# Kernel tuning notes

Hardware: AMD Instinct MI355X
Metric: run time of the kernel (lower is better)

The kernel has to match this reference:

```python
import jax, jax.numpy as jnp
import numpy as np
import math

B, C, A, W, H = 8, 128, 16, 64, 64


def setup_inputs() -> dict:
    key = jax.random.key(0)
    ks = jax.random.split(key, 7)
    s_in = 1.0 / math.sqrt(C)
    return {
        "x": jax.random.normal(ks[0], (B, C, W, H), dtype=jnp.float32),
        "Wq": jax.random.normal(ks[1], (A, C), dtype=jnp.float32) * s_in,
        "bq": jnp.zeros((A,), dtype=jnp.float32),
        "Wk": jax.random.normal(ks[2], (A, C), dtype=jnp.float32) * s_in,
        "bk": jnp.zeros((A,), dtype=jnp.float32),
        "Wv": jax.random.normal(ks[3], (C, C), dtype=jnp.float32) * s_in,
        "bv": jnp.zeros((C,), dtype=jnp.float32),
    }


def reference(x, Wq, bq, Wk, bk, Wv, bv):
    # 1x1 convs == per-pixel linear projections
    q = jnp.einsum('ac,bcwh->bawh', Wq, x) + bq[None, :, None, None]  # [B,A,W,H]
    k = jnp.einsum('ac,bcwh->bawh', Wk, x) + bk[None, :, None, None]  # [B,A,W,H]
    v = jnp.einsum('vc,bcwh->bvwh', Wv, x) + bv[None, :, None, None]  # [B,C,W,H]

    scale = 1.0 / math.sqrt(q.shape[1])
    # full spatial attention: [B, W, H, W, H]
    attn = jnp.einsum('bawh,baWH->bwhWH', q, k)
    b, w, h, _, _ = attn.shape
    attn = jax.nn.softmax(attn.reshape(b, w, h, -1) * scale, axis=-1)
    attn = attn.reshape(b, w, h, w, h)
    out = jnp.einsum('bwhWH,bvWH->bvwh', attn, v)  # [B,C,W,H]
    return out
```

## Files before the change

kernel.cpp:

```cpp
#include <hip/hip_runtime.h>
#include <math.h>

#define BB 8
#define CC 128
#define NN 4096

typedef _Float16 f16;
typedef _Float16 f16x4v __attribute__((ext_vector_type(4)));
typedef _Float16 f16x8 __attribute__((ext_vector_type(8)));
typedef float f32x4v __attribute__((ext_vector_type(4)));
typedef float f32x16 __attribute__((ext_vector_type(16)));

#if __has_builtin(__builtin_amdgcn_exp2f)
#define EXP2(x) __builtin_amdgcn_exp2f(x)
#else
#define EXP2(x) __expf((x)*0.69314718056f)
#endif

#define QSCALE 0.360673760222f
#define SHIFT  5.770780163555f

#define WF_BYTES 65536

__global__ __launch_bounds__(256)
void prep_kernel(const float* __restrict__ Wq, const float* __restrict__ bq,
                 const float* __restrict__ Wk, const float* __restrict__ bk,
                 const float* __restrict__ Wv, const float* __restrict__ bv,
                 f16* __restrict__ Wf, float* __restrict__ biasS)
{
    const int tg = blockIdx.x*256 + threadIdx.x;
    if (tg < 2560) {
        const int mt = tg >> 9, ks = (tg >> 6) & 7, l = tg & 63;
        const int n32 = l & 31, h = l >> 5;
        const int r = mt*32 + n32;
        f16x8 v8;
        #pragma unroll
        for (int i = 0; i < 8; i++) {
            int c = ks*16 + 8*h + i;
            float wv_;
            if (r < 16)      wv_ = QSCALE * Wq[r*CC + c];
            else if (r < 32) wv_ = Wk[(r-16)*CC + c];
            else             wv_ = Wv[(r-32)*CC + c];
            v8[i] = (f16)wv_;
        }
        *(f16x8*)&Wf[(size_t)tg*8] = v8;
    }
    if (blockIdx.x == 0 && threadIdx.x < 160) {
        int r = threadIdx.x;
        biasS[r] = r < 16 ? QSCALE*bq[r] : (r < 32 ? bk[r-16] : bv[r-32]);
    }
}

__global__ __launch_bounds__(256)
void proj_kernel(const float* __restrict__ x, const f16* __restrict__ Wf,
                 const float* __restrict__ biasS,
                 f16* __restrict__ Qt, f16* __restrict__ Kt, f16* __restrict__ Vf)
{
    __shared__ __align__(16) f16 Vl[CC*140];

    const int tid  = threadIdx.x;
    const int lane = tid & 63;
    const int wv   = tid >> 6;
    const int b    = blockIdx.x & 7;
    const int pt   = blockIdx.x >> 3;
    const int n32  = lane & 31;
    const int half = lane >> 5;
    const int p    = pt*128 + wv*32 + n32;

    const float* xp = x + (size_t)b*CC*NN + p;
    f16x8 xf[8];
    #pragma unroll
    for (int ks = 0; ks < 8; ks++) {
        float xv[8];
        #pragma unroll
        for (int i = 0; i < 8; i++)
            xv[i] = __builtin_nontemporal_load(&xp[(size_t)(ks*16 + 8*half + i)*NN]);
        #pragma unroll
        for (int i = 0; i < 8; i++) xf[ks][i] = (f16)xv[i];
    }

    f32x16 acc[5];
    #pragma unroll
    for (int mt = 0; mt < 5; mt++) acc[mt] = (f32x16)0.0f;
    #pragma unroll
    for (int ks = 0; ks < 8; ks++) {
        #pragma unroll
        for (int mt = 0; mt < 5; mt++) {
            f16x8 wfr = *(const f16x8*)&Wf[((size_t)(mt*8 + ks)*64 + lane)*8];
            acc[mt] = __builtin_amdgcn_mfma_f32_32x32x16_f16(wfr, xf[ks], acc[mt], 0, 0, 0);
        }
    }

    #pragma unroll
    for (int mt = 0; mt < 5; mt++) {
        #pragma unroll
        for (int q = 0; q < 4; q++) {
            float4 b4 = *(const float4*)&biasS[mt*32 + q*8 + 4*half];
            acc[mt][q*4+0] += b4.x; acc[mt][q*4+1] += b4.y;
            acc[mt][q*4+2] += b4.z; acc[mt][q*4+3] += b4.w;
        }
    }

    {
        size_t qkoff = ((size_t)b*NN + p)*16;
        f16x4v s0, s1, s2, s3;
        #pragma unroll
        for (int i = 0; i < 4; i++) {
            s0[i] = (f16)acc[0][i];    s1[i] = (f16)acc[0][4+i];
            s2[i] = (f16)acc[0][8+i];  s3[i] = (f16)acc[0][12+i];
        }
        *(f16x4v*)&Qt[qkoff + 4*half]     = s0;
        *(f16x4v*)&Qt[qkoff + 8 + 4*half] = s1;
        *(f16x4v*)&Kt[qkoff + 4*half]     = s2;
        *(f16x4v*)&Kt[qkoff + 8 + 4*half] = s3;
    }

    #pragma unroll
    for (int mt = 1; mt < 5; mt++) {
        #pragma unroll
        for (int g = 0; g < 16; g++) {
            int c = (mt-1)*32 + (g & 3) + 8*(g >> 2) + 4*half;
            Vl[c*140 + wv*32 + n32] = (f16)acc[mt][g];
        }
    }
    __syncthreads();

    #pragma unroll
    for (int pass = 0; pass < 8; pass++) {
        int item = pass*256 + tid;
        int l    = item & 63;
        int f    = (item >> 6) & 15;
        int ktl  = item >> 10;
        int c16  = f >> 2, ct = f & 3;
        int li   = l & 31, h2 = l >> 5;
        const f16* src = &Vl[(ct*32 + li)*140 + ktl*64 + c16*16 + 4*h2];
        f16x4v lo = *(const f16x4v*)&src[0];
        f16x4v hi = *(const f16x4v*)&src[8];
        f16x8 v8;
        #pragma unroll
        for (int i = 0; i < 4; i++) { v8[i] = lo[i]; v8[4+i] = hi[i]; }
        int ktg = pt*2 + ktl;
        *(f16x8*)&Vf[((((size_t)b*64 + ktg)*16 + c16*4 + ct)*64 + l)*8] = v8;
    }
}

__global__ __launch_bounds__(256, 2)
void attn_kernel(const f16* __restrict__ Qt, const f16* __restrict__ Kt,
                 const f16* __restrict__ Vf, float* __restrict__ out)
{
    __shared__ __align__(16) unsigned char lds_raw[53504];

    const int tid  = threadIdx.x;
    const int lane = tid & 63;
    const int w    = tid >> 6;
    const int cp   = w & 1;
    const int kh   = w >> 1;
    const int b    = blockIdx.x & 7;
    const int qt   = blockIdx.x >> 3;
    const int q0   = qt*64;
    const int n32  = lane & 31;
    const int half = lane >> 5;

    const f16* vb = Vf + (size_t)b*64*16*512;
    const f16* kb = Kt + (size_t)b*NN*16;
    const f16x8 qf = *(const f16x8*)&Qt[((size_t)b*NN + q0 + cp*32 + n32)*16 + half*8];

    f32x16 ofA[2], ofB[2];
    #pragma unroll
    for (int c = 0; c < 2; c++) { ofA[c] = (f32x16)0.0f; ofB[c] = (f32x16)0.0f; }
    float ps[4] = {0.f, 0.f, 0.f, 0.f};

    f16x8 kf0 = *(const f16x8*)&kb[((size_t)kh*64 + n32)*16 + half*8];
    f16x8 kf1 = *(const f16x8*)&kb[((size_t)kh*64 + 32 + n32)*16 + half*8];
    f16x8 vpf[8];
    {
        const f16* vt = vb + (size_t)kh*8192;
        #pragma unroll
        for (int kc = 0; kc < 4; kc++)
            #pragma unroll
            for (int j = 0; j < 2; j++)
                vpf[kc*2+j] = *(const f16x8*)&vt[((size_t)(kc*4 + 2*cp + j)*64 + lane)*8];
    }

    f16* Pex = (f16*)lds_raw;
    int pb = 0;

    for (int kt = kh; kt < NN/64; kt += 2) {
        const int ktn = (kt + 2 < NN/64) ? kt + 2 : kt;
        f16x8 kf0n = *(const f16x8*)&kb[((size_t)ktn*64 + n32)*16 + half*8];
        f16x8 kf1n = *(const f16x8*)&kb[((size_t)ktn*64 + 32 + n32)*16 + half*8];

        f16x8 po[4];
        {
            f32x16 St0 = __builtin_amdgcn_mfma_f32_32x32x16_f16(kf0, qf, (f32x16)(-SHIFT), 0, 0, 0);
            f32x16 St1 = __builtin_amdgcn_mfma_f32_32x32x16_f16(kf1, qf, (f32x16)(-SHIFT), 0, 0, 0);
            #pragma unroll
            for (int g = 0; g < 16; g++) {
                float e0 = EXP2(St0[g]); ps[g & 3] += e0; po[(g >> 3)][g & 7]     = (f16)e0;
                float e1 = EXP2(St1[g]); ps[g & 3] += e1; po[2 + (g >> 3)][g & 7] = (f16)e1;
            }
        }

        {
            f16* wr = &Pex[((size_t)(w*2 + pb)*4*64 + lane)*8];
            #pragma unroll
            for (int kc = 0; kc < 4; kc++)
                *(f16x8*)&wr[kc*512] = po[kc];
        }
        __syncthreads();
        f16x8 pq[4];
        {
            const f16* rd = &Pex[((size_t)((w^1)*2 + pb)*4*64 + lane)*8];
            #pragma unroll
            for (int kc = 0; kc < 4; kc++)
                pq[kc] = *(const f16x8*)&rd[kc*512];
        }

        const f16* vtn = vb + (size_t)ktn*8192;
#define PV_BLOCK(PA, PB)                                                              \
        _Pragma("unroll")                                                             \
        for (int kc = 0; kc < 4; kc++) {                                              \
            _Pragma("unroll")                                                         \
            for (int j = 0; j < 2; j++) {                                             \
                const int ii = kc*2 + j;                                              \
                f16x8 vc = vpf[ii];                                                   \
                vpf[ii] = *(const f16x8*)&vtn[((size_t)(kc*4 + 2*cp + j)*64 + lane)*8]; \
                ofA[j] = __builtin_amdgcn_mfma_f32_32x32x16_f16(PA[kc], vc, ofA[j], 0, 0, 0); \
                ofB[j] = __builtin_amdgcn_mfma_f32_32x32x16_f16(PB[kc], vc, ofB[j], 0, 0, 0); \
            }                                                                         \
        }
        if (cp == 0) { PV_BLOCK(po, pq) }
        else         { PV_BLOCK(pq, po) }
#undef PV_BLOCK

        kf0 = kf0n; kf1 = kf1n; pb ^= 1;
    }

    float ls = (ps[0] + ps[1]) + (ps[2] + ps[3]);
    ls += __shfl_xor(ls, 32);

    __syncthreads();
    if (w >= 2) {
        unsigned char* base = lds_raw + (size_t)cp*9216 + (size_t)lane*144;
        #pragma unroll
        for (int a = 0; a < 4; a++) {
            #pragma unroll
            for (int h = 0; h < 2; h++) {
                f16x8 t;
                #pragma unroll
                for (int jj = 0; jj < 8; jj++)
                    t[jj] = (f16)((a < 2 ? ofA[a & 1] : ofB[a & 1])[h*8 + jj]);
                *(f16x8*)(base + a*32 + h*16) = t;
            }
        }
        *(float*)(base + 128) = ls;
    }
    __syncthreads();
    if (w < 2) {
        unsigned char* base = lds_raw + (size_t)cp*9216 + (size_t)lane*144;
        #pragma unroll
        for (int a = 0; a < 4; a++) {
            #pragma unroll
            for (int h = 0; h < 2; h++) {
                f16x8 t = *(const f16x8*)(base + a*32 + h*16);
                #pragma unroll
                for (int jj = 0; jj < 8; jj++) {
                    float v = (float)t[jj];
                    if (a < 2) ofA[a & 1][h*8 + jj] += v;
                    else       ofB[a & 1][h*8 + jj] += v;
                }
            }
        }
        ls += *(const float*)(base + 128);
        float* ls_inv = (float*)(lds_raw + 18432);
        if (lane < 32) ls_inv[cp*32 + n32] = 1.f / ls;
    }
    __syncthreads();

    if (w < 2) {
        const float* ls_inv = (const float*)(lds_raw + 18432);
        float* Tb = (float*)(lds_raw + 18688);
        #pragma unroll
        for (int qts = 0; qts < 2; qts++) {
            #pragma unroll
            for (int j = 0; j < 4; j++) {
                f32x4v iv = *(const f32x4v*)&ls_inv[qts*32 + 8*j + 4*half];
                #pragma unroll
                for (int ctl = 0; ctl < 2; ctl++) {
                    const int c = (2*cp + ctl)*32 + n32;
                    f32x4v o;
                    #pragma unroll
                    for (int e = 0; e < 4; e++)
                        o[e] = (qts ? ofB[ctl] : ofA[ctl])[4*j + e] * iv[e];
                    *(f32x4v*)&Tb[(size_t)c*68 + qts*32 + 8*j + 4*half] = o;
                }
            }
        }
    }
    __syncthreads();
    {
        const float* Tb = (const float*)(lds_raw + 18688);
        #pragma unroll
        for (int it = 0; it < 8; it++) {
            int idx = it*256 + tid;
            int c = idx >> 4, qg = idx & 15;
            f32x4v v = *(const f32x4v*)&Tb[(size_t)c*68 + qg*4];
            __builtin_nontemporal_store(v,
                (f32x4v*)&out[((size_t)b*CC + c)*NN + q0 + qg*4]);
        }
    }
}

extern "C" void kernel_launch(void* const* d_in, const int* in_sizes, int n_in,
                              void* d_out, int out_size, void* d_ws, size_t ws_size,
                              hipStream_t stream) {
    const float* x  = (const float*)d_in[0];
    const float* Wq = (const float*)d_in[1];
    const float* bq = (const float*)d_in[2];
    const float* Wk = (const float*)d_in[3];
    const float* bk = (const float*)d_in[4];
    const float* Wv = (const float*)d_in[5];
    const float* bv = (const float*)d_in[6];
    float* out = (float*)d_out;

    f16* Qw = (f16*)d_ws;
    f16* Kw = Qw + (size_t)BB*NN*16;
    f16* Vw = Kw + (size_t)BB*NN*16;
    unsigned char* tail = (unsigned char*)d_out + (size_t)out_size*4 - WF_BYTES;
    f16*   Wf    = (f16*)tail;
    float* biasS = (float*)(tail + 49152);

    hipLaunchKernelGGL(prep_kernel, dim3(10), dim3(256), 0, stream,
                       Wq, bq, Wk, bk, Wv, bv, Wf, biasS);
    hipLaunchKernelGGL(proj_kernel, dim3(256), dim3(256), 0, stream,
                       x, Wf, biasS, Qw, Kw, Vw);
    hipLaunchKernelGGL(attn_kernel, dim3(512), dim3(256), 0, stream,
                       Qw, Kw, Vw, out);
}
```

Baseline: 133.9 us.

## Software-pipeline attention loop so PV MFMAs overlap next tile's exp

Restructures the main key-tile loop into a two-stage software pipeline. The QK MFMAs for the next tile are issued, then the PV MFMAs for the current tile run while those results land, and exp/pack/LDS exchange for the next tile follows. A prologue and epilogue handle the first and last tiles. The __syncthreads is replaced by an inline s_waitcnt lgkmcnt(0) plus s_barrier. The aim is to hide exp and MFMA latency and cut barrier overhead, at the cost of more live registers (double P buffers and K fragments), which could lower occupancy.

```diff
diff --git a/kernel.cpp b/kernel.cpp
--- a/kernel.cpp
+++ b/kernel.cpp
@@ -170,8 +170,12 @@
     for (int c = 0; c < 2; c++) { ofA[c] = (f32x16)0.0f; ofB[c] = (f32x16)0.0f; }
     float ps[4] = {0.f, 0.f, 0.f, 0.f};
 
-    f16x8 kf0 = *(const f16x8*)&kb[((size_t)kh*64 + n32)*16 + half*8];
-    f16x8 kf1 = *(const f16x8*)&kb[((size_t)kh*64 + 32 + n32)*16 + half*8];
+    f16* Pex = (f16*)lds_raw;
+
+    f16x8 kA0 = *(const f16x8*)&kb[((size_t)kh*64 + n32)*16 + half*8];
+    f16x8 kA1 = *(const f16x8*)&kb[((size_t)kh*64 + 32 + n32)*16 + half*8];
+    f16x8 kB0 = *(const f16x8*)&kb[((size_t)(kh+2)*64 + n32)*16 + half*8];
+    f16x8 kB1 = *(const f16x8*)&kb[((size_t)(kh+2)*64 + 32 + n32)*16 + half*8];
     f16x8 vpf[8];
     {
         const f16* vt = vb + (size_t)kh*8192;
@@ -182,59 +186,92 @@
                 vpf[kc*2+j] = *(const f16x8*)&vt[((size_t)(kc*4 + 2*cp + j)*64 + lane)*8];
     }
 
-    f16* Pex = (f16*)lds_raw;
-    int pb = 0;
-
-    for (int kt = kh; kt < NN/64; kt += 2) {
-        const int ktn = (kt + 2 < NN/64) ? kt + 2 : kt;
-        f16x8 kf0n = *(const f16x8*)&kb[((size_t)ktn*64 + n32)*16 + half*8];
-        f16x8 kf1n = *(const f16x8*)&kb[((size_t)ktn*64 + 32 + n32)*16 + half*8];
-
-        f16x8 po[4];
-        {
-            f32x16 St0 = __builtin_amdgcn_mfma_f32_32x32x16_f16(kf0, qf, (f32x16)(-SHIFT), 0, 0, 0);
-            f32x16 St1 = __builtin_amdgcn_mfma_f32_32x32x16_f16(kf1, qf, (f32x16)(-SHIFT), 0, 0, 0);
-            #pragma unroll
-            for (int g = 0; g < 16; g++) {
-                float e0 = EXP2(St0[g]); ps[g & 3] += e0; po[(g >> 3)][g & 7]     = (f16)e0;
-                float e1 = EXP2(St1[g]); ps[g & 3] += e1; po[2 + (g >> 3)][g & 7] = (f16)e1;
-            }
-        }
-
-        {
-            f16* wr = &Pex[((size_t)(w*2 + pb)*4*64 + lane)*8];
-            #pragma unroll
-            for (int kc = 0; kc < 4; kc++)
-                *(f16x8*)&wr[kc*512] = po[kc];
-        }
-        __syncthreads();
-        f16x8 pq[4];
-        {
-            const f16* rd = &Pex[((size_t)((w^1)*2 + pb)*4*64 + lane)*8];
-            #pragma unroll
-            for (int kc = 0; kc < 4; kc++)
-                pq[kc] = *(const f16x8*)&rd[kc*512];
-        }
-
-        const f16* vtn = vb + (size_t)ktn*8192;
-#define PV_BLOCK(PA, PB)                                                              \
+    f16x8 poA[4], pqA[4], poB[4], pqB[4];
+    {
+        f32x16 St0 = __builtin_amdgcn_mfma_f32_32x32x16_f16(kA0, qf, (f32x16)(-SHIFT), 0, 0, 0);
+        f32x16 St1 = __builtin_amdgcn_mfma_f32_32x32x16_f16(kA1, qf, (f32x16)(-SHIFT), 0, 0, 0);
+        #pragma unroll
+        for (int g = 0; g < 16; g++) {
+            float e0 = EXP2(St0[g]); ps[g & 3] += e0; poA[(g >> 3)][g & 7]     = (f16)e0;
+            float e1 = EXP2(St1[g]); ps[g & 3] += e1; poA[2 + (g >> 3)][g & 7] = (f16)e1;
+        }
+        f16* wr = &Pex[((size_t)(w*2 + 0)*4*64 + lane)*8];
+        #pragma unroll
+        for (int kc = 0; kc < 4; kc++) *(f16x8*)&wr[kc*512] = poA[kc];
+        asm volatile("s_waitcnt lgkmcnt(0)\n\ts_barrier" ::: "memory");
+        const f16* rd = &Pex[((size_t)((w^1)*2 + 0)*4*64 + lane)*8];
+        #pragma unroll
+        for (int kc = 0; kc < 4; kc++) pqA[kc] = *(const f16x8*)&rd[kc*512];
+    }
+
+#define PV_CORE(PA, PB, VTN)                                                          \
         _Pragma("unroll")                                                             \
         for (int kc = 0; kc < 4; kc++) {                                              \
             _Pragma("unroll")                                                         \
             for (int j = 0; j < 2; j++) {                                             \
                 const int ii = kc*2 + j;                                              \
                 f16x8 vc = vpf[ii];                                                   \
-                vpf[ii] = *(const f16x8*)&vtn[((size_t)(kc*4 + 2*cp + j)*64 + lane)*8]; \
+                vpf[ii] = *(const f16x8*)&(VTN)[((size_t)(kc*4 + 2*cp + j)*64 + lane)*8]; \
                 ofA[j] = __builtin_amdgcn_mfma_f32_32x32x16_f16(PA[kc], vc, ofA[j], 0, 0, 0); \
                 ofB[j] = __builtin_amdgcn_mfma_f32_32x32x16_f16(PB[kc], vc, ofB[j], 0, 0, 0); \
             }                                                                         \
         }
-        if (cp == 0) { PV_BLOCK(po, pq) }
-        else         { PV_BLOCK(pq, po) }
-#undef PV_BLOCK
-
-        kf0 = kf0n; kf1 = kf1n; pb ^= 1;
-    }
+
+#define STEP(KT_PV, PO_C, PQ_C, PO_N, PQ_N, KU0, KU1, KL0, KL1, PB)                   \
+    {                                                                                 \
+        const int tprep = (KT_PV) + 2;                                                \
+        f32x16 St0 = __builtin_amdgcn_mfma_f32_32x32x16_f16(KU0, qf, (f32x16)(-SHIFT), 0, 0, 0); \
+        f32x16 St1 = __builtin_amdgcn_mfma_f32_32x32x16_f16(KU1, qf, (f32x16)(-SHIFT), 0, 0, 0); \
+        {                                                                             \
+            int tl = tprep + 2; if (tl >= NN/64) tl = tprep;                          \
+            KL0 = *(const f16x8*)&kb[((size_t)tl*64 + n32)*16 + half*8];              \
+            KL1 = *(const f16x8*)&kb[((size_t)tl*64 + 32 + n32)*16 + half*8];         \
+        }                                                                             \
+        const f16* vtn = vb + (size_t)tprep*8192;                                     \
+        if (cp == 0) { PV_CORE(PO_C, PQ_C, vtn) } else { PV_CORE(PQ_C, PO_C, vtn) }   \
+        _Pragma("unroll")                                                             \
+        for (int g = 0; g < 16; g++) {                                                \
+            float e0 = EXP2(St0[g]); ps[g & 3] += e0; PO_N[(g >> 3)][g & 7]     = (f16)e0; \
+            float e1 = EXP2(St1[g]); ps[g & 3] += e1; PO_N[2 + (g >> 3)][g & 7] = (f16)e1; \
+        }                                                                             \
+        {                                                                             \
+            f16* wr = &Pex[((size_t)(w*2 + (PB))*4*64 + lane)*8];                     \
+            _Pragma("unroll")                                                         \
+            for (int kc = 0; kc < 4; kc++) *(f16x8*)&wr[kc*512] = PO_N[kc];           \
+        }                                                                             \
+        asm volatile("s_waitcnt lgkmcnt(0)\n\ts_barrier" ::: "memory");               \
+        {                                                                             \
+            const f16* rd = &Pex[((size_t)((w^1)*2 + (PB))*4*64 + lane)*8];           \
+            _Pragma("unroll")                                                         \
+            for (int kc = 0; kc < 4; kc++) PQ_N[kc] = *(const f16x8*)&rd[kc*512];     \
+        }                                                                             \
+    }
+
+    for (int it = 0; it < 15; ++it) {
+        const int kt = kh + it*4;
+        STEP(kt,   poA, pqA, poB, pqB, kB0, kB1, kA0, kA1, 1)
+        STEP(kt+2, poB, pqB, poA, pqA, kA0, kA1, kB0, kB1, 0)
+    }
+    STEP(kh+60, poA, pqA, poB, pqB, kB0, kB1, kA0, kA1, 1)
+    {
+        #pragma unroll
+        for (int kc = 0; kc < 4; kc++) {
+            #pragma unroll
+            for (int j = 0; j < 2; j++) {
+                const int ii = kc*2 + j;
+                f16x8 vc = vpf[ii];
+                if (cp == 0) {
+                    ofA[j] = __builtin_amdgcn_mfma_f32_32x32x16_f16(poB[kc], vc, ofA[j], 0, 0, 0);
+                    ofB[j] = __builtin_amdgcn_mfma_f32_32x32x16_f16(pqB[kc], vc, ofB[j], 0, 0, 0);
+                } else {
+                    ofA[j] = __builtin_amdgcn_mfma_f32_32x32x16_f16(pqB[kc], vc, ofA[j], 0, 0, 0);
+                    ofB[j] = __builtin_amdgcn_mfma_f32_32x32x16_f16(poB[kc], vc, ofB[j], 0, 0, 0);
+                }
+            }
+        }
+    }
+#undef STEP
+#undef PV_CORE
 
     float ls = (ps[0] + ps[1]) + (ps[2] + ps[3]);
     ls += __shfl_xor(ls, 32);
```

Result: slower. 160.9 us (+20.1%).
